# Optimization experiments

Hardware: AMD Instinct MI355X
Metric: run time of the kernel (lower is better)

Reference implementation:

```python
import jax, jax.numpy as jnp
import numpy as np

# Synthetic forest: T complete B-ary trees of depth D.
# Nodes stored level-major in `embeds`: level 0 (roots) first, then level 1, ...
# Level l has T*B**l nodes; children of node j at level l are rows j*B..j*B+B-1 of level l+1.
T_TREES, BRANCH, DEPTH = 16, 4, 8
IN_DIM, HIDDEN, N_LABEL = 128, 128, 5


def _level_layout():
    counts = [T_TREES * BRANCH ** l for l in range(DEPTH)]
    offsets = np.concatenate([[0], np.cumsum(counts)]).astype(np.int64)
    return counts, offsets


def setup_inputs() -> dict:
    key = jax.random.key(0)
    counts, offsets = _level_layout()
    n_total = int(offsets[-1])
    ks = jax.random.split(key, 16)
    s_in = 1.0 / np.sqrt(IN_DIM)
    s_h = 1.0 / np.sqrt(HIDDEN)
    d = {"embeds": jax.random.normal(ks[0], (n_total, IN_DIM), dtype=jnp.float32)}
    # gate params: *x linears have bias, *h linears are bias-free (as in torch module)
    d["Wix"] = jax.random.uniform(ks[1], (HIDDEN, IN_DIM), jnp.float32, -s_in, s_in)
    d["bix"] = jax.random.uniform(ks[2], (HIDDEN,), jnp.float32, -s_in, s_in)
    d["Wih"] = jax.random.uniform(ks[3], (HIDDEN, HIDDEN), jnp.float32, -s_h, s_h)
    d["Wfx"] = jax.random.uniform(ks[4], (HIDDEN, IN_DIM), jnp.float32, -s_in, s_in)
    d["bfx"] = jax.random.uniform(ks[5], (HIDDEN,), jnp.float32, -s_in, s_in)
    d["Wfh"] = jax.random.uniform(ks[6], (HIDDEN, HIDDEN), jnp.float32, -s_h, s_h)
    d["Wox"] = jax.random.uniform(ks[7], (HIDDEN, IN_DIM), jnp.float32, -s_in, s_in)
    d["box"] = jax.random.uniform(ks[8], (HIDDEN,), jnp.float32, -s_in, s_in)
    d["Woh"] = jax.random.uniform(ks[9], (HIDDEN, HIDDEN), jnp.float32, -s_h, s_h)
    d["Wux"] = jax.random.uniform(ks[10], (HIDDEN, IN_DIM), jnp.float32, -s_in, s_in)
    d["bux"] = jax.random.uniform(ks[11], (HIDDEN,), jnp.float32, -s_in, s_in)
    d["Wuh"] = jax.random.uniform(ks[12], (HIDDEN, HIDDEN), jnp.float32, -s_h, s_h)
    d["Wout"] = 0.01 * jax.random.normal(ks[13], (N_LABEL, HIDDEN), dtype=jnp.float32)
    d["bout"] = 0.01 * jax.random.normal(ks[14], (N_LABEL,), dtype=jnp.float32)
    return d


def reference(embeds, Wix, bix, Wih, Wfx, bfx, Wfh, Wox, box, Woh, Wux, bux, Wuh, Wout, bout):
    counts, offsets = _level_layout()
    H, B = HIDDEN, BRANCH
    child_h = child_c = None
    # leaves-first (level = DEPTH-1 .. 0), matching `while level >= 0` order
    for level in range(DEPTH - 1, -1, -1):
        n = counts[level]
        o = int(offsets[level])
        x = embeds[o:o + n]  # [n, in_dim] == index_select of this level's nodes
        if child_h is None:  # leaves: zero child state
            h_sum = jnp.zeros((n, H), embeds.dtype)
            fc_sum = jnp.zeros((n, H), embeds.dtype)
        else:
            # child-sum over the B children gathered from the previous level
            h_sum = child_h.reshape(n, B, H).sum(axis=1)  # child_h_sum
            fh = child_h @ Wfh.T  # [n*B, H]
            fx = jnp.repeat(x, B, axis=0) @ Wfx.T + bfx  # parent embed per child
            f = jax.nn.sigmoid(fx + fh)
            fc_sum = (f * child_c).reshape(n, B, H).sum(axis=1)  # child_fc_sum
        i = jax.nn.sigmoid(x @ Wix.T + bix + h_sum @ Wih.T)
        og = jax.nn.sigmoid(x @ Wox.T + box + h_sum @ Woh.T)
        u = jnp.tanh(x @ Wux.T + bux + h_sum @ Wuh.T)
        c = i * u + fc_sum
        h = og * jnp.tanh(c)
        child_c, child_h = c, h
    # output head at the root level (dropout is identity at eval)
    return child_h @ Wout.T + bout  # [T_TREES, N_LABEL]
```

## Files before the change

### kernel.cpp

```cpp
#include <hip/hip_runtime.h>
#include <hip/hip_bf16.h>


#define HID 128

typedef unsigned short u16;
typedef unsigned int u32;
typedef __attribute__((ext_vector_type(8))) short short8;
typedef __attribute__((ext_vector_type(4))) float floatx4;

__device__ __forceinline__ float bf2f(u16 u) {
  union { unsigned int u; float f; } v; v.u = ((unsigned int)u) << 16; return v.f;
}
__device__ __forceinline__ u16 f2bf(float f) {
  __hip_bfloat16 b = __float2bfloat16(f);
  return *reinterpret_cast<u16*>(&b);
}
__device__ __forceinline__ short8 f2bf8(float4 f0, float4 f1) {
  short8 s;
  s[0] = (short)f2bf(f0.x); s[1] = (short)f2bf(f0.y);
  s[2] = (short)f2bf(f0.z); s[3] = (short)f2bf(f0.w);
  s[4] = (short)f2bf(f1.x); s[5] = (short)f2bf(f1.y);
  s[6] = (short)f2bf(f1.z); s[7] = (short)f2bf(f1.w);
  return s;
}
__device__ __forceinline__ float sigm(float x) {
  return __builtin_amdgcn_rcpf(1.0f + __expf(-x));
}
__device__ __forceinline__ float tanh_fast(float x) {
  float ax = fabsf(x);
  float e = __expf(2.0f * ax);
  float t = 1.0f - 2.0f * __builtin_amdgcn_rcpf(e + 1.0f);
  return copysignf(t, x);
}

__global__ void prep_weights(const float* __restrict__ Wix, const float* __restrict__ Wih,
                             const float* __restrict__ Wfx, const float* __restrict__ Wfh,
                             const float* __restrict__ Wox, const float* __restrict__ Woh,
                             const float* __restrict__ Wux, const float* __restrict__ Wuh,
                             u16* __restrict__ Wcat, u16* __restrict__ Wfxb, u16* __restrict__ Wfhb)
{
  int t = blockIdx.x * 256 + threadIdx.x;
  if (t < 98304) {
    int nrow = t >> 8, k = t & 255;
    int gate = nrow >> 7, r = nrow & 127;
    float v;
    if (k < 128) {
      const float* W = (gate == 0) ? Wix : (gate == 1) ? Wox : Wux;
      v = W[r * 128 + k];
    } else {
      const float* W = (gate == 0) ? Wih : (gate == 1) ? Woh : Wuh;
      v = W[r * 128 + (k - 128)];
    }
    Wcat[t] = f2bf(v);
  } else if (t < 98304 + 16384) {
    int i = t - 98304;
    Wfxb[i] = f2bf(Wfx[i]);
  } else if (t < 98304 + 32768) {
    int i = t - 98304 - 16384;
    Wfhb[i] = f2bf(Wfh[i]);
  }
}

template <int MODE>
__global__ __launch_bounds__(512, 2)
void tree_kernel(const float* __restrict__ embeds,
                 const u16* __restrict__ Wcat,
                 const u16* __restrict__ Wfxb,
                 const u16* __restrict__ Wfhb,
                 const float* __restrict__ bix, const float* __restrict__ bfx,
                 const float* __restrict__ box, const float* __restrict__ bux,
                 u16* __restrict__ hf, float* __restrict__ fc_buf,
                 int noff, int poff)
{
  constexpr bool HASC = (MODE >= 1);
  constexpr int OFF_SHS  = 16384;
  constexpr int OFF_SXP  = OFF_SHS + (HASC ? 16384 : 0);
  constexpr int OFF_SFXP = OFF_SXP + 4096;
  constexpr int SMEM_SZ  = OFF_SFXP + 16 * 132 * 4;
  __shared__ char smem[SMEM_SZ];
  u16*   sx   = (u16*)smem;
  u16*   shs  = (u16*)(smem + OFF_SHS);
  u16*   sxp  = (u16*)(smem + OFF_SXP);
  float* sfxp = (float*)(smem + OFF_SFXP);

  const int tid  = threadIdx.x;
  const int wave = tid >> 6;
  const int lane = tid & 63;
  const int lg   = lane >> 4;
  const int ln   = lane & 15;
  const int pbase = blockIdx.x * 64;
  const int col  = wave * 16 + ln;
  const int prow0 = poff + (pbase >> 2);

  {
    int row = tid >> 3;
    int k0  = (tid & 7) * 16;
    const float* src = embeds + (size_t)(noff + pbase + row) * HID + k0;
    unsigned sw = ((unsigned)(row & 7)) << 4;
    char* dst = (char*)sx + row * 256;
    float4 f0 = *(const float4*)src;
    float4 f1 = *(const float4*)(src + 4);
    float4 f2 = *(const float4*)(src + 8);
    float4 f3 = *(const float4*)(src + 12);
    *(short8*)(dst + (((unsigned)(k0 * 2)) ^ sw))      = f2bf8(f0, f1);
    *(short8*)(dst + (((unsigned)(k0 * 2 + 16)) ^ sw)) = f2bf8(f2, f3);
  }
  if constexpr (HASC) {
    int row = tid >> 3, cg = tid & 7;
    const u16* src = hf + (size_t)(noff + pbase + row) * HID + cg * 16;
    short8 v0 = *(const short8*)src;
    short8 v1 = *(const short8*)(src + 8);
    unsigned sw = ((unsigned)(row & 7)) << 4;
    char* dst = (char*)shs + row * 256;
    *(short8*)(dst + ((cg * 32) ^ sw))      = v0;
    *(short8*)(dst + ((cg * 32 + 16) ^ sw)) = v1;
  }
  {
    if (tid < 128) {
      int row = tid >> 3;
      int k0  = (tid & 7) * 16;
      const float* src = embeds + (size_t)(prow0 + row) * HID + k0;
      unsigned sw = ((unsigned)(row & 7)) << 4;
      char* dst = (char*)sxp + row * 256;
      float4 f0 = *(const float4*)src;
      float4 f1 = *(const float4*)(src + 4);
      float4 f2 = *(const float4*)(src + 8);
      float4 f3 = *(const float4*)(src + 12);
      *(short8*)(dst + (((unsigned)(k0 * 2)) ^ sw))      = f2bf8(f0, f1);
      *(short8*)(dst + (((unsigned)(k0 * 2 + 16)) ^ sw)) = f2bf8(f2, f3);
    }
  }
  __syncthreads();

  float fcown[4][4];
  if constexpr (HASC) {
#pragma unroll
    for (int m = 0; m < 4; ++m)
#pragma unroll
      for (int r = 0; r < 4; ++r)
        fcown[m][r] = fc_buf[(size_t)(noff + pbase + m * 16 + lg * 4 + r) * HID + col];
  }

  floatx4 acc[4][3] = {};
  constexpr int KT = HASC ? 8 : 4;
#pragma unroll
  for (int kt = 0; kt < KT; ++kt) {
    short8 a[4];
#pragma unroll
    for (int m = 0; m < 4; ++m) {
      int row = m * 16 + ln;
      unsigned sw = ((unsigned)(row & 7)) << 4;
      const char* base = (kt < 4) ? (const char*)sx : (const char*)shs;
      int kb = ((kt & 3) * 32 + lg * 8) * 2;
      a[m] = *(const short8*)(base + row * 256 + (((unsigned)kb) ^ sw));
    }
#pragma unroll
    for (int g = 0; g < 3; ++g) {
      short8 b = *(const short8*)(Wcat + (size_t)((g * 8 + wave) * 16 + ln) * 256 + kt * 32 + lg * 8);
#pragma unroll
      for (int m = 0; m < 4; ++m)
        acc[m][g] = __builtin_amdgcn_mfma_f32_16x16x32_bf16(a[m], b, acc[m][g], 0, 0, 0);
    }
  }

  {
    floatx4 accxp = {};
#pragma unroll
    for (int kt = 0; kt < 4; ++kt) {
      short8 b = *(const short8*)(Wfxb + (size_t)(wave * 16 + ln) * HID + kt * 32 + lg * 8);
      unsigned sw = ((unsigned)(ln & 7)) << 4;
      short8 a = *(const short8*)((char*)sxp + ln * 256 +
                                  (((unsigned)((kt * 32 + lg * 8) * 2)) ^ sw));
      accxp = __builtin_amdgcn_mfma_f32_16x16x32_bf16(a, b, accxp, 0, 0, 0);
    }
#pragma unroll
    for (int r = 0; r < 4; ++r)
      sfxp[(lg * 4 + r) * 132 + col] = accxp[r];
  }
  __syncthreads();

  float cv[4][4];
  {
    float bi = bix[col], bo = box[col], bu = bux[col];
#pragma unroll
    for (int m = 0; m < 4; ++m) {
      float hs4 = 0.f;
#pragma unroll
      for (int r = 0; r < 4; ++r) {
        int row = m * 16 + lg * 4 + r;
        float iv = sigm(acc[m][0][r] + bi);
        float ov = sigm(acc[m][1][r] + bo);
        float uv = tanh_fast(acc[m][2][r] + bu);
        float fcv = HASC ? fcown[m][r] : 0.f;
        float c = iv * uv + fcv;
        float hv = ov * tanh_fast(c);
        cv[m][r] = c;
        hs4 += hv;
        unsigned sw = ((unsigned)(row & 7)) << 4;
        *(u16*)((char*)sx + row * 256 + (((unsigned)(col * 2)) ^ sw)) = f2bf(hv);
      }
      hf[(size_t)(prow0 + m * 4 + lg) * HID + col] = f2bf(hs4);
    }
  }

  {
    __syncthreads();
    floatx4 ah[4] = {};
#pragma unroll
    for (int kt = 0; kt < 4; ++kt) {
      short8 b = *(const short8*)(Wfhb + (size_t)(wave * 16 + ln) * HID + kt * 32 + lg * 8);
#pragma unroll
      for (int m = 0; m < 4; ++m) {
        int row = m * 16 + ln;
        unsigned sw = ((unsigned)(row & 7)) << 4;
        short8 a = *(const short8*)((char*)sx + row * 256 +
                                    (((unsigned)((kt * 32 + lg * 8) * 2)) ^ sw));
        ah[m] = __builtin_amdgcn_mfma_f32_16x16x32_bf16(a, b, ah[m], 0, 0, 0);
      }
    }
    float bf = bfx[col];
#pragma unroll
    for (int m = 0; m < 4; ++m) {
      float fxv = sfxp[(m * 4 + lg) * 132 + col] + bf;
      float s = 0.f;
#pragma unroll
      for (int r = 0; r < 4; ++r)
        s += sigm(fxv + ah[m][r]) * cv[m][r];
      fc_buf[(size_t)(prow0 + m * 4 + lg) * HID + col] = s;
    }
  }
}

__global__ __launch_bounds__(512, 2)
void fused_tail(const float* __restrict__ embeds,
                const u16* __restrict__ Wcat,
                const u16* __restrict__ Wfxb,
                const u16* __restrict__ Wfhb,
                const float* __restrict__ bix, const float* __restrict__ bfx,
                const float* __restrict__ box, const float* __restrict__ bux,
                const float* __restrict__ Wout, const float* __restrict__ bout,
                u16* __restrict__ hf, float* __restrict__ fc_buf,
                float* __restrict__ out)
{
  __shared__ char smem[16384 + 16384 + 16 * 132 * 4];
  u16*   sx   = (u16*)smem;
  u16*   shs  = (u16*)(smem + 16384);
  float* sfxp = (float*)(smem + 32768);

  const int tid  = threadIdx.x;
  const int wave = tid >> 6;
  const int lane = tid & 63;
  const int lg   = lane >> 4;
  const int ln   = lane & 15;
  const int col  = wave * 16 + ln;
  const int b    = blockIdx.x;

  const int offs[3] = {0, 16, 80};

#pragma unroll 1
  for (int l = 2; l >= 0; --l) {
    const int nrows = 64 >> (2 * (2 - l));
    const int noff  = offs[l] + b * nrows;
    const bool last = (l == 0);
    const int poff  = last ? 0 : offs[l - 1] + b * (nrows >> 2);

    {
      int row = tid >> 3;
      int k0  = (tid & 7) * 16;
      const float* src = embeds + (size_t)(noff + row) * HID + k0;
      unsigned sw = ((unsigned)(row & 7)) << 4;
      char* dst = (char*)sx + row * 256;
      float4 f0 = *(const float4*)src;
      float4 f1 = *(const float4*)(src + 4);
      float4 f2 = *(const float4*)(src + 8);
      float4 f3 = *(const float4*)(src + 12);
      *(short8*)(dst + (((unsigned)(k0 * 2)) ^ sw))      = f2bf8(f0, f1);
      *(short8*)(dst + (((unsigned)(k0 * 2 + 16)) ^ sw)) = f2bf8(f2, f3);
    }
    {
      int row = tid >> 3, cg = tid & 7;
      const u16* src = hf + (size_t)(noff + row) * HID + cg * 16;
      short8 v0 = *(const short8*)src;
      short8 v1 = *(const short8*)(src + 8);
      unsigned sw = ((unsigned)(row & 7)) << 4;
      char* dst = (char*)shs + row * 256;
      *(short8*)(dst + ((cg * 32) ^ sw))      = v0;
      *(short8*)(dst + ((cg * 32 + 16) ^ sw)) = v1;
    }
    __syncthreads();

    float fcown[4][4];
#pragma unroll
    for (int m = 0; m < 4; ++m)
#pragma unroll
      for (int r = 0; r < 4; ++r)
        fcown[m][r] = fc_buf[(size_t)(noff + m * 16 + lg * 4 + r) * HID + col];

    floatx4 acc[4][3] = {};
#pragma unroll
    for (int kt = 0; kt < 8; ++kt) {
      short8 a[4];
#pragma unroll
      for (int m = 0; m < 4; ++m) {
        int row = m * 16 + ln;
        unsigned sw = ((unsigned)(row & 7)) << 4;
        const char* base = (kt < 4) ? (const char*)sx : (const char*)shs;
        int kb = ((kt & 3) * 32 + lg * 8) * 2;
        a[m] = *(const short8*)(base + row * 256 + (((unsigned)kb) ^ sw));
      }
#pragma unroll
      for (int g = 0; g < 3; ++g) {
        short8 bb = *(const short8*)(Wcat + (size_t)((g * 8 + wave) * 16 + ln) * 256 + kt * 32 + lg * 8);
#pragma unroll
        for (int m = 0; m < 4; ++m)
          acc[m][g] = __builtin_amdgcn_mfma_f32_16x16x32_bf16(a[m], bb, acc[m][g], 0, 0, 0);
      }
    }

    if (!last) {
      floatx4 accxp = {};
      const float* xprow = embeds + (size_t)(poff + ln) * HID;
#pragma unroll
      for (int kt = 0; kt < 4; ++kt) {
        short8 bb = *(const short8*)(Wfxb + (size_t)(wave * 16 + ln) * HID + kt * 32 + lg * 8);
        float4 f0 = *(const float4*)(xprow + kt * 32 + lg * 8);
        float4 f1 = *(const float4*)(xprow + kt * 32 + lg * 8 + 4);
        accxp = __builtin_amdgcn_mfma_f32_16x16x32_bf16(f2bf8(f0, f1), bb, accxp, 0, 0, 0);
      }
#pragma unroll
      for (int r = 0; r < 4; ++r)
        sfxp[(lg * 4 + r) * 132 + col] = accxp[r];
    }
    __syncthreads();

    float cv[4][4];
    {
      float bi = bix[col], bo = box[col], bu = bux[col];
#pragma unroll
      for (int m = 0; m < 4; ++m) {
        float hs4 = 0.f;
#pragma unroll
        for (int r = 0; r < 4; ++r) {
          int row = m * 16 + lg * 4 + r;
          if (row < nrows) {
            float iv = sigm(acc[m][0][r] + bi);
            float ov = sigm(acc[m][1][r] + bo);
            float uv = tanh_fast(acc[m][2][r] + bu);
            float c = iv * uv + fcown[m][r];
            float hv = ov * tanh_fast(c);
            cv[m][r] = c;
            hs4 += hv;
            unsigned sw = ((unsigned)(row & 7)) << 4;
            *(u16*)((char*)sx + row * 256 + (((unsigned)(col * 2)) ^ sw)) = f2bf(hv);
          }
        }
        if (!last && (m * 4 + lg) < (nrows >> 2))
          hf[(size_t)(poff + m * 4 + lg) * HID + col] = f2bf(hs4);
      }
    }

    if (!last) {
      __syncthreads();
      floatx4 ah[4] = {};
#pragma unroll
      for (int kt = 0; kt < 4; ++kt) {
        short8 bb = *(const short8*)(Wfhb + (size_t)(wave * 16 + ln) * HID + kt * 32 + lg * 8);
#pragma unroll
        for (int m = 0; m < 4; ++m) {
          int row = m * 16 + ln;
          unsigned sw = ((unsigned)(row & 7)) << 4;
          short8 a = *(const short8*)((char*)sx + row * 256 +
                                      (((unsigned)((kt * 32 + lg * 8) * 2)) ^ sw));
          ah[m] = __builtin_amdgcn_mfma_f32_16x16x32_bf16(a, bb, ah[m], 0, 0, 0);
        }
      }
      float bf = bfx[col];
#pragma unroll
      for (int m = 0; m < 4; ++m) {
        if ((m * 4 + lg) < (nrows >> 2)) {
          float fxv = sfxp[(m * 4 + lg) * 132 + col] + bf;
          float s = 0.f;
#pragma unroll
          for (int r = 0; r < 4; ++r)
            s += sigm(fxv + ah[m][r]) * cv[m][r];
          fc_buf[(size_t)(poff + m * 4 + lg) * HID + col] = s;
        }
      }
    }
    __syncthreads();
  }

  if (tid < 20) {
    int r = tid / 5, lbl = tid - r * 5;
    unsigned sw = ((unsigned)r) << 4;
    float s = bout[lbl];
    const float* wr = Wout + lbl * 128;
    const char* hrow = (const char*)sx + r * 256;
#pragma unroll 4
    for (int k = 0; k < 128; ++k)
      s += bf2f(*(const u16*)(hrow + (((unsigned)(k * 2)) ^ sw))) * wr[k];
    out[(4 * b + r) * 5 + lbl] = s;
  }
}

extern "C" void kernel_launch(void* const* d_in, const int* in_sizes, int n_in,
                              void* d_out, int out_size, void* d_ws, size_t ws_size,
                              hipStream_t stream)
{
  const float* embeds = (const float*)d_in[0];
  const float* Wix = (const float*)d_in[1];
  const float* bix = (const float*)d_in[2];
  const float* Wih = (const float*)d_in[3];
  const float* Wfx = (const float*)d_in[4];
  const float* bfx = (const float*)d_in[5];
  const float* Wfh = (const float*)d_in[6];
  const float* Wox = (const float*)d_in[7];
  const float* box = (const float*)d_in[8];
  const float* Woh = (const float*)d_in[9];
  const float* Wux = (const float*)d_in[10];
  const float* bux = (const float*)d_in[11];
  const float* Wuh = (const float*)d_in[12];
  const float* Wout = (const float*)d_in[13];
  const float* bout = (const float*)d_in[14];

  static const int counts[8]  = {16, 64, 256, 1024, 4096, 16384, 65536, 262144};
  static const int offsets[9] = {0, 16, 80, 336, 1360, 5456, 21840, 87376, 349520};

  char* ws = (char*)d_ws;
  u16*   hf     = (u16*)ws;
  float* fc_buf = (float*)(ws + 89477120);
  u16*   Wcat   = (u16*)(ws + 89477120 + 178954240);
  u16*   Wfxb   = Wcat + 384 * 256;
  u16*   Wfhb   = Wfxb + 128 * 128;

  prep_weights<<<512, 256, 0, stream>>>(Wix, Wih, Wfx, Wfh, Wox, Woh, Wux, Wuh,
                                        Wcat, Wfxb, Wfhb);

  tree_kernel<0><<<262144 / 64, 512, 0, stream>>>(
      embeds, Wcat, Wfxb, Wfhb, bix, bfx, box, bux,
      hf, fc_buf, 87376, 21840);

  for (int l = 6; l >= 3; --l) {
    int nl = counts[l];
    tree_kernel<1><<<nl / 64, 512, 0, stream>>>(
        embeds, Wcat, Wfxb, Wfhb, bix, bfx, box, bux,
        hf, fc_buf, offsets[l], offsets[l - 1]);
  }

  fused_tail<<<4, 512, 0, stream>>>(
      embeds, Wcat, Wfxb, Wfhb, bix, bfx, box, bux,
      Wout, bout, hf, fc_buf, (float*)d_out);
}
```

Baseline: 245.6 us.

## Pack child h-sum and fc-sum into one bf16-pair interleaved buffer

Replaces the separate bf16 h-sum buffer and fp32 fc-sum buffer with a single u32 buffer that holds both values as bf16 (fc in the high half, h in the low half). Each parent entry is written with one store instead of two, and the fc-sum is stored at reduced precision, which cuts the fc-sum bytes in half. The h-sum load now reads 4-byte words and extracts the low halves, so it pulls in the interleaved fc data too. Rounding the cell-state sum to bf16 may add numerical error.

New measurement: 270.7 us. 10.2% more time.

```diff
diff --git a/kernel.cpp b/kernel.cpp
--- a/kernel.cpp
+++ b/kernel.cpp
@@ -8,6 +8,7 @@
 typedef unsigned int u32;
 typedef __attribute__((ext_vector_type(8))) short short8;
 typedef __attribute__((ext_vector_type(4))) float floatx4;
+typedef __attribute__((ext_vector_type(4))) unsigned int u32x4;
 
 __device__ __forceinline__ float bf2f(u16 u) {
   union { unsigned int u; float f; } v; v.u = ((unsigned int)u) << 16; return v.f;
@@ -70,7 +71,7 @@
                  const u16* __restrict__ Wfhb,
                  const float* __restrict__ bix, const float* __restrict__ bfx,
                  const float* __restrict__ box, const float* __restrict__ bux,
-                 u16* __restrict__ hf, float* __restrict__ fc_buf,
+                 u32* __restrict__ chs,
                  int noff, int poff)
 {
   constexpr bool HASC = (MODE >= 1);
@@ -108,9 +109,19 @@
   }
   if constexpr (HASC) {
     int row = tid >> 3, cg = tid & 7;
-    const u16* src = hf + (size_t)(noff + pbase + row) * HID + cg * 16;
-    short8 v0 = *(const short8*)src;
-    short8 v1 = *(const short8*)(src + 8);
+    const u32* src = chs + (size_t)(noff + pbase + row) * HID + cg * 16;
+    u32x4 p0 = *(const u32x4*)src;
+    u32x4 p1 = *(const u32x4*)(src + 4);
+    u32x4 p2 = *(const u32x4*)(src + 8);
+    u32x4 p3 = *(const u32x4*)(src + 12);
+    short8 v0, v1;
+#pragma unroll
+    for (int j = 0; j < 4; ++j) {
+      v0[j]     = (short)(u16)(p0[j] & 0xFFFFu);
+      v0[4 + j] = (short)(u16)(p1[j] & 0xFFFFu);
+      v1[j]     = (short)(u16)(p2[j] & 0xFFFFu);
+      v1[4 + j] = (short)(u16)(p3[j] & 0xFFFFu);
+    }
     unsigned sw = ((unsigned)(row & 7)) << 4;
     char* dst = (char*)shs + row * 256;
     *(short8*)(dst + ((cg * 32) ^ sw))      = v0;
@@ -138,8 +149,10 @@
 #pragma unroll
     for (int m = 0; m < 4; ++m)
 #pragma unroll
-      for (int r = 0; r < 4; ++r)
-        fcown[m][r] = fc_buf[(size_t)(noff + pbase + m * 16 + lg * 4 + r) * HID + col];
+      for (int r = 0; r < 4; ++r) {
+        u32 p = chs[(size_t)(noff + pbase + m * 16 + lg * 4 + r) * HID + col];
+        fcown[m][r] = bf2f((u16)(p >> 16));
+      }
   }
 
   floatx4 acc[4][3] = {};
@@ -181,11 +194,12 @@
   __syncthreads();
 
   float cv[4][4];
+  float hs4[4];
   {
     float bi = bix[col], bo = box[col], bu = bux[col];
 #pragma unroll
     for (int m = 0; m < 4; ++m) {
-      float hs4 = 0.f;
+      float hs = 0.f;
 #pragma unroll
       for (int r = 0; r < 4; ++r) {
         int row = m * 16 + lg * 4 + r;
@@ -196,11 +210,11 @@
         float c = iv * uv + fcv;
         float hv = ov * tanh_fast(c);
         cv[m][r] = c;
-        hs4 += hv;
+        hs += hv;
         unsigned sw = ((unsigned)(row & 7)) << 4;
         *(u16*)((char*)sx + row * 256 + (((unsigned)(col * 2)) ^ sw)) = f2bf(hv);
       }
-      hf[(size_t)(prow0 + m * 4 + lg) * HID + col] = f2bf(hs4);
+      hs4[m] = hs;
     }
   }
 
@@ -227,7 +241,8 @@
 #pragma unroll
       for (int r = 0; r < 4; ++r)
         s += sigm(fxv + ah[m][r]) * cv[m][r];
-      fc_buf[(size_t)(prow0 + m * 4 + lg) * HID + col] = s;
+      u32 packed = ((u32)f2bf(s) << 16) | (u32)f2bf(hs4[m]);
+      chs[(size_t)(prow0 + m * 4 + lg) * HID + col] = packed;
     }
   }
 }
@@ -240,7 +255,7 @@
                 const float* __restrict__ bix, const float* __restrict__ bfx,
                 const float* __restrict__ box, const float* __restrict__ bux,
                 const float* __restrict__ Wout, const float* __restrict__ bout,
-                u16* __restrict__ hf, float* __restrict__ fc_buf,
+                u32* __restrict__ chs,
                 float* __restrict__ out)
 {
   __shared__ char smem[16384 + 16384 + 16 * 132 * 4];
@@ -280,9 +295,19 @@
     }
     {
       int row = tid >> 3, cg = tid & 7;
-      const u16* src = hf + (size_t)(noff + row) * HID + cg * 16;
-      short8 v0 = *(const short8*)src;
-      short8 v1 = *(const short8*)(src + 8);
+      const u32* src = chs + (size_t)(noff + row) * HID + cg * 16;
+      u32x4 p0 = *(const u32x4*)src;
+      u32x4 p1 = *(const u32x4*)(src + 4);
+      u32x4 p2 = *(const u32x4*)(src + 8);
+      u32x4 p3 = *(const u32x4*)(src + 12);
+      short8 v0, v1;
+#pragma unroll
+      for (int j = 0; j < 4; ++j) {
+        v0[j]     = (short)(u16)(p0[j] & 0xFFFFu);
+        v0[4 + j] = (short)(u16)(p1[j] & 0xFFFFu);
+        v1[j]     = (short)(u16)(p2[j] & 0xFFFFu);
+        v1[4 + j] = (short)(u16)(p3[j] & 0xFFFFu);
+      }
       unsigned sw = ((unsigned)(row & 7)) << 4;
       char* dst = (char*)shs + row * 256;
       *(short8*)(dst + ((cg * 32) ^ sw))      = v0;
@@ -294,8 +319,10 @@
 #pragma unroll
     for (int m = 0; m < 4; ++m)
 #pragma unroll
-      for (int r = 0; r < 4; ++r)
-        fcown[m][r] = fc_buf[(size_t)(noff + m * 16 + lg * 4 + r) * HID + col];
+      for (int r = 0; r < 4; ++r) {
+        u32 p = chs[(size_t)(noff + m * 16 + lg * 4 + r) * HID + col];
+        fcown[m][r] = bf2f((u16)(p >> 16));
+      }
 
     floatx4 acc[4][3] = {};
 #pragma unroll
@@ -335,11 +362,12 @@
     __syncthreads();
 
     float cv[4][4];
+    float hs4[4];
     {
       float bi = bix[col], bo = box[col], bu = bux[col];
 #pragma unroll
       for (int m = 0; m < 4; ++m) {
-        float hs4 = 0.f;
+        float hs = 0.f;
 #pragma unroll
         for (int r = 0; r < 4; ++r) {
           int row = m * 16 + lg * 4 + r;
@@ -350,13 +378,12 @@
             float c = iv * uv + fcown[m][r];
             float hv = ov * tanh_fast(c);
             cv[m][r] = c;
-            hs4 += hv;
+            hs += hv;
             unsigned sw = ((unsigned)(row & 7)) << 4;
             *(u16*)((char*)sx + row * 256 + (((unsigned)(col * 2)) ^ sw)) = f2bf(hv);
           }
         }
-        if (!last && (m * 4 + lg) < (nrows >> 2))
-          hf[(size_t)(poff + m * 4 + lg) * HID + col] = f2bf(hs4);
+        hs4[m] = hs;
       }
     }
 
@@ -384,7 +411,8 @@
 #pragma unroll
           for (int r = 0; r < 4; ++r)
             s += sigm(fxv + ah[m][r]) * cv[m][r];
-          fc_buf[(size_t)(poff + m * 4 + lg) * HID + col] = s;
+          u32 packed = ((u32)f2bf(s) << 16) | (u32)f2bf(hs4[m]);
+          chs[(size_t)(poff + m * 4 + lg) * HID + col] = packed;
         }
       }
     }
@@ -428,27 +456,26 @@
   static const int offsets[9] = {0, 16, 80, 336, 1360, 5456, 21840, 87376, 349520};
 
   char* ws = (char*)d_ws;
-  u16*   hf     = (u16*)ws;
-  float* fc_buf = (float*)(ws + 89477120);
-  u16*   Wcat   = (u16*)(ws + 89477120 + 178954240);
-  u16*   Wfxb   = Wcat + 384 * 256;
-  u16*   Wfhb   = Wfxb + 128 * 128;
+  u32* chs  = (u32*)ws;
+  u16* Wcat = (u16*)(ws + 178954240);
+  u16* Wfxb = Wcat + 384 * 256;
+  u16* Wfhb = Wfxb + 128 * 128;
 
   prep_weights<<<512, 256, 0, stream>>>(Wix, Wih, Wfx, Wfh, Wox, Woh, Wux, Wuh,
                                         Wcat, Wfxb, Wfhb);
 
   tree_kernel<0><<<262144 / 64, 512, 0, stream>>>(
       embeds, Wcat, Wfxb, Wfhb, bix, bfx, box, bux,
-      hf, fc_buf, 87376, 21840);
+      chs, 87376, 21840);
 
   for (int l = 6; l >= 3; --l) {
     int nl = counts[l];
     tree_kernel<1><<<nl / 64, 512, 0, stream>>>(
         embeds, Wcat, Wfxb, Wfhb, bix, bfx, box, bux,
-        hf, fc_buf, offsets[l], offsets[l - 1]);
+        chs, offsets[l], offsets[l - 1]);
   }
 
   fused_tail<<<4, 512, 0, stream>>>(
       embeds, Wcat, Wfxb, Wfhb, bix, bfx, box, bux,
-      Wout, bout, hf, fc_buf, (float*)d_out);
-}
+      Wout, bout, chs, (float*)d_out);
+}
```
